# Optimization experiments

Hardware: AMD Instinct MI355X
Metric: run time of the kernel (lower is better)

Reference implementation:

```python
import jax, jax.numpy as jnp
import numpy as np

S, B, E, H = 192, 2, 512, 2
D = E // H      # head_dim = 256 == E/2; required so attn_fc(3*D) matches concat of three E/2 chunks
BH = B * H

def _lin(x, W, b):
    return x @ W.T + b

def setup_inputs():
    key = jax.random.key(0)
    ks = jax.random.split(key, 16)
    p = lambda k, *s: jax.random.normal(k, s, jnp.float32) * 0.02
    return {
        "query":       jax.random.normal(ks[0], (S, B, E), jnp.float32),
        "entity":      jax.random.normal(ks[1], (S, B, E), jnp.float32),
        "ex_entity":   jax.random.normal(ks[2], (S, B, B, E), jnp.float32),
        "ex_relation": jax.random.normal(ks[3], (S, B, B, E), jnp.float32),
        "Wq": p(ks[4], D, E), "bq": jnp.zeros((D,), jnp.float32),
        "Wk": p(ks[5], D, E), "bk": jnp.zeros((D,), jnp.float32),
        "Wv": p(ks[6], D, E), "bv": jnp.zeros((D,), jnp.float32),
        "We": p(ks[7], D, E), "be": jnp.zeros((D,), jnp.float32),
        "Wxe": p(ks[8], D, E), "bxe": jnp.zeros((D,), jnp.float32),
        "Wxr": p(ks[9], D, E), "bxr": jnp.zeros((D,), jnp.float32),
        "Wa": p(ks[10], 1, 3 * D), "ba": jnp.zeros((1,), jnp.float32),
        "Wo": p(ks[11], E, E), "bo": jnp.zeros((E,), jnp.float32),
    }

def reference(query, entity, ex_entity, ex_relation,
              Wq, bq, Wk, bk, Wv, bv, We, be, Wxe, bxe, Wxr, bxr, Wa, ba, Wo, bo):
    e = _lin(entity, We, be)            # [S,B,D]
    q = _lin(query, Wq, bq)             # [S,B,D]
    exr = _lin(ex_entity, Wxe, bxe)     # exent_proj(ex_entity) -> [S,B,B,D]
    exe = _lin(ex_relation, Wxr, bxr)   # exrel_proj(ex_relation) -> [S,B,B,D]
    e_b = jnp.broadcast_to(e[:, :, None, :], exe.shape)
    exz = jnp.concatenate([exe, e_b, exr], axis=-1)                              # [S,B,B,3D]
    exw = jax.nn.softmax(jax.nn.leaky_relu((exz @ Wa.T + ba)[..., 0]), axis=-1)  # [S,B,B]
    we = jnp.einsum('sbk,skd->sbd', exw, e)  # torch.bmm; dead when en_tgt==tgt (faithful fwd compute)
    del we
    qe = jnp.concatenate([q, e], axis=-1)    # [S,B,E]  (else-branch: e.size(0)==q.size(0))
    k = _lin(query, Wk, bk)
    v = _lin(query, Wv, bv)
    ke = jnp.concatenate([k, e], axis=-1)
    ve = jnp.concatenate([v, e], axis=-1)
    shp = lambda x: jnp.swapaxes(x.reshape(S, BH, D), 0, 1)  # torch _shape -> [BH,S,D]
    qe_s, ke_s, ve_s = shp(qe), shp(ke), shp(ve)
    # edge[i,j,b,:] = entity[i,b] - entity[j,b]; torch then does a flat .view(BH,S,S,D)
    edge = (entity[:, None] - entity[None, :]).reshape(BH, S, S, D)
    # qe: transpose(0,1).repeat(S,1,1,1).transpose(0,1).reshape -> broadcast over src then flat reshape
    qe_r = jnp.broadcast_to(jnp.swapaxes(qe_s, 0, 1)[:, None], (S, S, BH, D)).reshape(BH, S, S, D)
    # ke: repeat(S,1,1,1).reshape (flat)
    ke_r = jnp.broadcast_to(ke_s[None], (S, BH, S, D)).reshape(BH, S, S, D)
    z = jnp.concatenate([qe_r, ke_r, edge], axis=-1)                             # [BH,S,S,3D]
    aw = jax.nn.softmax(jax.nn.leaky_relu((z @ Wa.T + ba)[..., 0]), axis=-1)     # [BH,S,S]
    out = jnp.einsum('bts,bsd->btd', aw, ve_s)                                   # [BH,S,D]
    out = jnp.swapaxes(out, 0, 1).reshape(S, B, E)
    return _lin(out, Wo, bo)
```

## Files before the change

### kernel.cpp

```cpp
#include <hip/hip_runtime.h>
#include <math.h>


#define SS 192
#define WTV 0
#define WTE 131072
#define WTO 262144
#define TO  524288
#define VO  526592
#define EO  624896
#define OO  723200

__device__ __forceinline__ float wave_reduce_add(float p) {
    #pragma unroll
    for (int off = 32; off >= 1; off >>= 1) p += __shfl_xor(p, off, 64);
    return p;
}

__global__ __launch_bounds__(1024) void k_prep(
    const float* __restrict__ Wv, const float* __restrict__ We,
    const float* __restrict__ Wo, float* __restrict__ ws)
{
    int o = blockIdx.x * 1024 + threadIdx.x;
    const float4* src; float4* dst; int idx; int D;
    if (o < 32768)      { src = (const float4*)Wv; dst = (float4*)(ws + WTV); idx = o;         D = 256; }
    else if (o < 65536) { src = (const float4*)We; dst = (float4*)(ws + WTE); idx = o - 32768; D = 256; }
    else                { src = (const float4*)Wo; dst = (float4*)(ws + WTO); idx = o - 65536; D = 512; }
    int d  = idx >> 7;
    int k4 = idx & 127;
    dst[k4 * D + d] = src[idx];
}

__global__ __launch_bounds__(1024) void k_proj(
    const float* __restrict__ query, const float* __restrict__ entity,
    const float* __restrict__ Wq, const float* __restrict__ bq,
    const float* __restrict__ Wk, const float* __restrict__ bk,
    const float* __restrict__ bv, const float* __restrict__ We,
    const float* __restrict__ be, const float* __restrict__ Wa,
    float* __restrict__ ws)
{
    __shared__ __align__(16) float shb[8192];
    __shared__ __align__(16) float uo[516];
    int blk = blockIdx.x;
    int tid = threadIdx.x;
    int wv   = __builtin_amdgcn_readfirstlane(tid >> 6);
    int lane = tid & 63;

    if (blk < 384) {
        int m   = blk / 192;
        int rem = blk % 192;
        int dh  = rem / 96;
        int rg  = rem % 96;
        int r0  = rg * 4;
        int d0  = dh * 128;
        int kc  = __builtin_amdgcn_readfirstlane(tid >> 7);
        int dl  = tid & 127;
        const float*  A    = m ? entity : query;
        const float*  bias = m ? be : bv;
        const float4* WT   = (const float4*)(ws + (m ? WTE : WTV));
        float*        dst  = ws + (m ? EO : VO);
        const float4* A4   = (const float4*)A;

        float acc[4];
        #pragma unroll
        for (int r = 0; r < 4; r++) acc[r] = 0.f;

        int k4b = kc * 16;
        #pragma unroll 8
        for (int i = 0; i < 16; i++) {
            int k4 = k4b + i;
            float4 w = WT[k4 * 256 + d0 + dl];
            #pragma unroll
            for (int r = 0; r < 4; r++) {
                float4 a = A4[(r0 + r) * 128 + k4];
                acc[r] += a.x * w.x + a.y * w.y + a.z * w.z + a.w * w.w;
            }
        }
        #pragma unroll
        for (int r = 0; r < 4; r++) shb[kc * 512 + r * 128 + dl] = acc[r];
        __syncthreads();
        if (tid < 512) {
            int r = tid >> 7, d2 = tid & 127;
            float v = 0.f;
            #pragma unroll
            for (int k = 0; k < 8; k++) v += shb[k * 512 + r * 128 + d2];
            dst[(size_t)(r0 + r) * 256 + d0 + d2] = v + bias[d0 + d2];
        }
        return;
    }

    if (blk < 392) {
        float* red = shb;
        int tab = blk - 384;
        int p   = (tab < 4) ? tab : tab - 4;
        int b   = p >> 1, h = p & 1;
        const float* wa   = Wa + ((tab < 4) ? 0 : 256);
        const float* W    = h ? We : ((tab < 4) ? Wq : Wk);
        const float* bias = h ? be : ((tab < 4) ? bq : bk);
        const float* x    = h ? entity : query;

        float u8[8];
        #pragma unroll
        for (int i = 0; i < 8; i++) u8[i] = 0.f;
        #pragma unroll 4
        for (int dd = 0; dd < 16; dd++) {
            int d = wv * 16 + dd;
            float wad = wa[d];
            const float4* Wr = (const float4*)(W + (size_t)d * 512);
            float4 w0 = Wr[lane * 2], w1 = Wr[lane * 2 + 1];
            u8[0] += wad * w0.x; u8[1] += wad * w0.y; u8[2] += wad * w0.z; u8[3] += wad * w0.w;
            u8[4] += wad * w1.x; u8[5] += wad * w1.y; u8[6] += wad * w1.z; u8[7] += wad * w1.w;
        }
        if (wv < 8) {
            #pragma unroll
            for (int i = 0; i < 8; i++) red[wv * 512 + lane * 8 + i] = u8[i];
        }
        __syncthreads();
        if (wv >= 8) {
            #pragma unroll
            for (int i = 0; i < 8; i++)
                atomicAdd(&red[(wv - 8) * 512 + lane * 8 + i], u8[i]);
        }
        __syncthreads();
        if (tid < 512) {
            float s = 0.f;
            #pragma unroll
            for (int w = 0; w < 8; w++) s += red[w * 512 + tid];
            uo[tid] = s;
        }
        __syncthreads();
        if (tid < 256) red[tid] = wa[tid] * bias[tid];
        __syncthreads();
        for (int o = 128; o >= 1; o >>= 1) {
            if (tid < o) red[tid] += red[tid + o];
            __syncthreads();
        }
        float off = red[0];

        const float4* u4 = (const float4*)uo;
        float4 ua = u4[lane * 2], ub = u4[lane * 2 + 1];
        for (int rr = 0; rr < 12; rr++) {
            int r = wv * 12 + rr;
            const float4* xr = (const float4*)(x + (size_t)(r * 2 + b) * 512);
            float4 a0 = xr[lane * 2], a1 = xr[lane * 2 + 1];
            float pp = a0.x*ua.x + a0.y*ua.y + a0.z*ua.z + a0.w*ua.w
                     + a1.x*ub.x + a1.y*ub.y + a1.z*ub.z + a1.w*ub.w;
            pp = wave_reduce_add(pp);
            if (lane == 0) ws[TO + tab * SS + r] = pp + off;
        }
        return;
    }

    {
        int m = blk - 392;
        float4 wa4 = ((const float4*)(Wa + 512))[lane];
        for (int rr = 0; rr < 12; rr++) {
            int i = wv * 12 + rr;
            const float4* er = (const float4*)(entity
                + (size_t)(i * 2 + (m >> 1)) * 512 + (m & 1) * 256);
            float4 e4 = er[lane];
            float pp = e4.x*wa4.x + e4.y*wa4.y + e4.z*wa4.z + e4.w*wa4.w;
            pp = wave_reduce_add(pp);
            if (lane == 0) ws[TO + (8 + m) * SS + i] = pp;
        }
    }
}

__global__ __launch_bounds__(1024) void k_attn(
    const float* __restrict__ ba_p, float* __restrict__ ws)
{
    __shared__ __align__(16) float pl[4096];
    __shared__ __align__(16) float sp4[768];
    int blk = blockIdx.x;
    int bh  = blk & 3;
    int rem2 = blk >> 2;
    int tg  = rem2 % 48;
    int dhf = rem2 / 48;
    int b = bh >> 1, h = bh & 1;
    const float* T = ws + TO;
    float ba = ba_p[0];
    int tid  = threadIdx.x;
    int wv   = __builtin_amdgcn_readfirstlane(tid >> 6);
    int lane = tid & 63;

    if (wv < 4) {
        int ti = wv;
        int i_idx = bh * 48 + tg;
        float sc[3]; float mx = -1e30f;
        #pragma unroll
        for (int i = 0; i < 3; i++) {
            int s_ = lane + 64 * i;
            int m  = s_ & 3;
            int j  = ti * 48 + (s_ >> 2);
            float xv = T[m * SS + i_idx] + T[(4 + ti) * SS + s_]
                     + T[(8 + m) * SS + i_idx] - T[(8 + m) * SS + j] + ba;
            xv = (xv >= 0.f) ? xv : 0.01f * xv;
            sc[i] = xv; mx = fmaxf(mx, xv);
        }
        #pragma unroll
        for (int o = 32; o >= 1; o >>= 1) mx = fmaxf(mx, __shfl_xor(mx, o, 64));
        float sum = 0.f;
        #pragma unroll
        for (int i = 0; i < 3; i++) { sc[i] = __expf(sc[i] - mx); sum += sc[i]; }
        sum = wave_reduce_add(sum);
        float inv = 1.f / sum;
        #pragma unroll
        for (int i = 0; i < 3; i++) sp4[ti * SS + lane + 64 * i] = sc[i] * inv;
    }
    __syncthreads();

    int sq = __builtin_amdgcn_readfirstlane(tid >> 7);
    int dl = tid & 127;
    int dd = dhf * 128 + dl;
    const float* src = ws + (h ? EO : VO) + b * 256 + dd;
    float a[4] = {0.f, 0.f, 0.f, 0.f};
    int s0 = sq * 24;
    #pragma unroll 8
    for (int s2 = 0; s2 < 24; s2++) {
        int s = s0 + s2;
        float xv = src[(size_t)s * 512];
        #pragma unroll
        for (int ti = 0; ti < 4; ti++) a[ti] += sp4[ti * SS + s] * xv;
    }
    #pragma unroll
    for (int ti = 0; ti < 4; ti++) pl[sq * 512 + ti * 128 + dl] = a[ti];
    __syncthreads();
    if (tid < 512) {
        int ti = tid >> 7, d2 = tid & 127;
        float v = 0.f;
        #pragma unroll
        for (int k = 0; k < 8; k++) v += pl[k * 512 + ti * 128 + d2];
        int t = tg * 4 + ti;
        ws[OO + (size_t)(2 * t + b) * 512 + h * 256 + dhf * 128 + d2] = v;
    }
}

__global__ __launch_bounds__(1024) void k_out(
    const float* __restrict__ bo, const float* __restrict__ ws,
    float* __restrict__ out)
{
    __shared__ float pl[4096];
    int blk = blockIdx.x;
    int rg  = blk >> 2;
    int cg  = blk & 3;
    int r0  = rg * 4;
    int c0  = cg * 128;
    int tid = threadIdx.x;
    int kc  = __builtin_amdgcn_readfirstlane(tid >> 7);
    int cl  = tid & 127;
    const float4* A4 = (const float4*)(ws + OO);
    const float4* WT = (const float4*)(ws + WTO);

    float acc[4];
    #pragma unroll
    for (int r = 0; r < 4; r++) acc[r] = 0.f;

    int k4b = kc * 16;
    #pragma unroll 8
    for (int i = 0; i < 16; i++) {
        int k4 = k4b + i;
        float4 w = WT[(size_t)k4 * 512 + c0 + cl];
        #pragma unroll
        for (int r = 0; r < 4; r++) {
            float4 a = A4[(r0 + r) * 128 + k4];
            acc[r] += a.x * w.x + a.y * w.y + a.z * w.z + a.w * w.w;
        }
    }
    #pragma unroll
    for (int r = 0; r < 4; r++) pl[kc * 512 + r * 128 + cl] = acc[r];
    __syncthreads();
    if (tid < 512) {
        int r = tid >> 7, c2 = tid & 127;
        float v = 0.f;
        #pragma unroll
        for (int k = 0; k < 8; k++) v += pl[k * 512 + r * 128 + c2];
        out[(size_t)(r0 + r) * 512 + c0 + c2] = v + bo[c0 + c2];
    }
}

extern "C" void kernel_launch(void* const* d_in, const int* in_sizes, int n_in,
                              void* d_out, int out_size, void* d_ws, size_t ws_size,
                              hipStream_t stream) {
    const float* query  = (const float*)d_in[0];
    const float* entity = (const float*)d_in[1];
    const float* Wq = (const float*)d_in[4];  const float* bq = (const float*)d_in[5];
    const float* Wk = (const float*)d_in[6];  const float* bk = (const float*)d_in[7];
    const float* Wv = (const float*)d_in[8];  const float* bv = (const float*)d_in[9];
    const float* We = (const float*)d_in[10]; const float* be = (const float*)d_in[11];
    const float* Wa = (const float*)d_in[16]; const float* ba = (const float*)d_in[17];
    const float* Wo = (const float*)d_in[18]; const float* bo = (const float*)d_in[19];
    float* ws  = (float*)d_ws;
    float* out = (float*)d_out;

    hipLaunchKernelGGL(k_prep, dim3(128), dim3(1024), 0, stream, Wv, We, Wo, ws);
    hipLaunchKernelGGL(k_proj, dim3(396), dim3(1024), 0, stream,
                       query, entity, Wq, bq, Wk, bk, bv, We, be, Wa, ws);
    hipLaunchKernelGGL(k_attn, dim3(384), dim3(1024), 0, stream, ba, ws);
    hipLaunchKernelGGL(k_out,  dim3(384), dim3(1024), 0, stream, bo, ws, out);
}
```

Before: 48.14 us.

## Fuse weight-transpose prep into projection kernel via shared-memory tiled transpose

Removes the separate k_prep launch. The V/E projection blocks now load Wv/We rows directly and transpose them on the fly through padded shared memory in k-chunks, with each block covering 8 rows instead of 4. The Wo transpose moves into extra blocks of the same launch. This saves one kernel launch and a global round-trip for the transposed Wv/We, at the cost of extra __syncthreads per chunk and fewer projection blocks.

```diff
diff --git a/kernel.cpp b/kernel.cpp
--- a/kernel.cpp
+++ b/kernel.cpp
@@ -3,8 +3,6 @@
 
 
 #define SS 192
-#define WTV 0
-#define WTE 131072
 #define WTO 262144
 #define TO  524288
 #define VO  526592
@@ -17,81 +15,90 @@
     return p;
 }
 
-__global__ __launch_bounds__(1024) void k_prep(
-    const float* __restrict__ Wv, const float* __restrict__ We,
-    const float* __restrict__ Wo, float* __restrict__ ws)
-{
-    int o = blockIdx.x * 1024 + threadIdx.x;
-    const float4* src; float4* dst; int idx; int D;
-    if (o < 32768)      { src = (const float4*)Wv; dst = (float4*)(ws + WTV); idx = o;         D = 256; }
-    else if (o < 65536) { src = (const float4*)We; dst = (float4*)(ws + WTE); idx = o - 32768; D = 256; }
-    else                { src = (const float4*)Wo; dst = (float4*)(ws + WTO); idx = o - 65536; D = 512; }
-    int d  = idx >> 7;
-    int k4 = idx & 127;
-    dst[k4 * D + d] = src[idx];
-}
-
-__global__ __launch_bounds__(1024) void k_proj(
+__global__ __launch_bounds__(1024) void k_projprep(
     const float* __restrict__ query, const float* __restrict__ entity,
     const float* __restrict__ Wq, const float* __restrict__ bq,
     const float* __restrict__ Wk, const float* __restrict__ bk,
-    const float* __restrict__ bv, const float* __restrict__ We,
-    const float* __restrict__ be, const float* __restrict__ Wa,
+    const float* __restrict__ Wv, const float* __restrict__ bv,
+    const float* __restrict__ We, const float* __restrict__ be,
+    const float* __restrict__ Wa, const float* __restrict__ Wo,
     float* __restrict__ ws)
 {
-    __shared__ __align__(16) float shb[8192];
+    __shared__ __align__(16) float shb[8448];
     __shared__ __align__(16) float uo[516];
     int blk = blockIdx.x;
     int tid = threadIdx.x;
     int wv   = __builtin_amdgcn_readfirstlane(tid >> 6);
     int lane = tid & 63;
 
-    if (blk < 384) {
-        int m   = blk / 192;
-        int rem = blk % 192;
-        int dh  = rem / 96;
-        int rg  = rem % 96;
-        int r0  = rg * 4;
+    if (blk < 192) {
+        int m   = blk / 96;
+        int rem = blk % 96;
+        int dh  = rem / 48;
+        int rg  = rem % 48;
+        int r0  = rg * 8;
         int d0  = dh * 128;
-        int kc  = __builtin_amdgcn_readfirstlane(tid >> 7);
+        int q   = __builtin_amdgcn_readfirstlane(tid >> 7);
         int dl  = tid & 127;
+        const float4* Wsrc = (const float4*)(m ? We : Wv);
+        const float*  bias = m ? be : bv;
         const float*  A    = m ? entity : query;
-        const float*  bias = m ? be : bv;
-        const float4* WT   = (const float4*)(ws + (m ? WTE : WTV));
         float*        dst  = ws + (m ? EO : VO);
         const float4* A4   = (const float4*)A;
-
-        float acc[4];
-        #pragma unroll
-        for (int r = 0; r < 4; r++) acc[r] = 0.f;
-
-        int k4b = kc * 16;
-        #pragma unroll 8
-        for (int i = 0; i < 16; i++) {
-            int k4 = k4b + i;
-            float4 w = WT[k4 * 256 + d0 + dl];
-            #pragma unroll
-            for (int r = 0; r < 4; r++) {
-                float4 a = A4[(r0 + r) * 128 + k4];
-                acc[r] += a.x * w.x + a.y * w.y + a.z * w.z + a.w * w.w;
+        float4* WL = (float4*)shb;
+
+        float acc[8];
+        #pragma unroll
+        for (int r = 0; r < 8; r++) acc[r] = 0.f;
+
+        for (int c = 0; c < 8; c++) {
+            #pragma unroll
+            for (int j = 0; j < 2; j++) {
+                int idx  = tid + j * 1024;
+                int dloc = idx >> 4;
+                int k4l  = idx & 15;
+                WL[k4l * 129 + dloc] =
+                    Wsrc[(size_t)(d0 + dloc) * 128 + c * 16 + k4l];
             }
-        }
-        #pragma unroll
-        for (int r = 0; r < 4; r++) shb[kc * 512 + r * 128 + dl] = acc[r];
-        __syncthreads();
-        if (tid < 512) {
+            __syncthreads();
+            #pragma unroll
+            for (int j = 0; j < 2; j++) {
+                int k4l = q * 2 + j;
+                float4 w = WL[k4l * 129 + dl];
+                int k4 = c * 16 + k4l;
+                #pragma unroll
+                for (int r = 0; r < 8; r++) {
+                    float4 a = A4[(size_t)(r0 + r) * 128 + k4];
+                    acc[r] += a.x * w.x + a.y * w.y + a.z * w.z + a.w * w.w;
+                }
+            }
+            __syncthreads();
+        }
+        float* part = shb;
+        #pragma unroll
+        for (int r = 0; r < 8; r++) part[q * 1024 + r * 128 + dl] = acc[r];
+        __syncthreads();
+        {
             int r = tid >> 7, d2 = tid & 127;
             float v = 0.f;
             #pragma unroll
-            for (int k = 0; k < 8; k++) v += shb[k * 512 + r * 128 + d2];
+            for (int k = 0; k < 8; k++) v += part[k * 1024 + r * 128 + d2];
             dst[(size_t)(r0 + r) * 256 + d0 + d2] = v + bias[d0 + d2];
         }
         return;
     }
 
-    if (blk < 392) {
+    if (blk < 256) {
+        int o  = (blk - 192) * 1024 + tid;
+        int c  = o >> 7;
+        int k4 = o & 127;
+        ((float4*)(ws + WTO))[k4 * 512 + c] = ((const float4*)Wo)[o];
+        return;
+    }
+
+    if (blk < 264) {
         float* red = shb;
-        int tab = blk - 384;
+        int tab = blk - 256;
         int p   = (tab < 4) ? tab : tab - 4;
         int b   = p >> 1, h = p & 1;
         const float* wa   = Wa + ((tab < 4) ? 0 : 256);
@@ -152,7 +159,7 @@
     }
 
     {
-        int m = blk - 392;
+        int m = blk - 264;
         float4 wa4 = ((const float4*)(Wa + 512))[lane];
         for (int rr = 0; rr < 12; rr++) {
             int i = wv * 12 + rr;
@@ -292,9 +299,8 @@
     float* ws  = (float*)d_ws;
     float* out = (float*)d_out;
 
-    hipLaunchKernelGGL(k_prep, dim3(128), dim3(1024), 0, stream, Wv, We, Wo, ws);
-    hipLaunchKernelGGL(k_proj, dim3(396), dim3(1024), 0, stream,
-                       query, entity, Wq, bq, Wk, bk, bv, We, be, Wa, ws);
+    hipLaunchKernelGGL(k_projprep, dim3(268), dim3(1024), 0, stream,
+                       query, entity, Wq, bq, Wk, bk, Wv, bv, We, be, Wa, Wo, ws);
     hipLaunchKernelGGL(k_attn, dim3(384), dim3(1024), 0, stream, ba, ws);
     hipLaunchKernelGGL(k_out,  dim3(384), dim3(1024), 0, stream, bo, ws, out);
 }
```

New measurement: 40.23 us, median of 3. -16.4%, faster.
